# Kernel optimization log

Measured on AMD Instinct MI355X. Metric: run time of the kernel, lower is better.

Reference implementation:

```python
import jax, jax.numpy as jnp
import numpy as np

BLOCK_NUM = 64
B, M, K, N = 4, 4096, 4096, 4096  # batch, rows, in_features, out_features


def setup_inputs() -> dict:
    key = jax.random.key(0)
    k1, k2 = jax.random.split(key)
    x = jax.random.normal(k1, (B, M, K), dtype=jnp.float32)
    weight = jax.random.normal(k2, (K, N), dtype=jnp.float32) * 0.02
    return {"x": x, "weight": weight}


def reference(x, weight):
    # Block-local matmul: output block (i, j) = A_block(i, j) @ W_block(i, j).
    # No cross-block reduction: each (i, j) output block depends on exactly one
    # A block and one W block. Vectorized as a single einsum over all blocks.
    b, m, k = x.shape
    k2, n = weight.shape
    Bn = BLOCK_NUM
    r, c, o = m // Bn, k // Bn, n // Bn  # per-block rows / contract / cols
    A = x.reshape(b, Bn, r, Bn, c)        # [b, i, r, j, c]
    W = weight.reshape(Bn, c, Bn, o)      # [i, c, j, o] (rows split by i, cols by j)
    out = jnp.einsum('birjc,icjo->birjo', A, W)
    return out.reshape(b, m, n)
```

## Files before the change

### kernel.cpp

```cpp
#include <hip/hip_runtime.h>
#include <hip/hip_bf16.h>


typedef short bf16x8 __attribute__((ext_vector_type(8)));
typedef float f32x4 __attribute__((ext_vector_type(4)));

__device__ __forceinline__ unsigned short f2bf(float f) {
    union { float f; unsigned int u; } v; v.f = f;
    unsigned int u = v.u;
    u += 0x7fffu + ((u >> 16) & 1u);
    return (unsigned short)(u >> 16);
}

__global__ __launch_bounds__(256, 4) void block_matmul_kernel(
    const float* __restrict__ x, const float* __restrict__ w,
    float* __restrict__ out) {
    __shared__ unsigned short As[64 * 64];
    __shared__ unsigned short Ws[64 * 64];

    const int nwg   = 4 * 64 * 64;
    const int chunk = nwg >> 3;
    int orig = blockIdx.x;
    int wg   = (orig & 7) * chunk + (orig >> 3);

    int b  = wg & 3;
    int ij = wg >> 2;
    int i  = ij >> 6;
    int j  = ij & 63;

    const float* Ab = x   + ((size_t)b * 4096 + (size_t)i * 64) * 4096 + (size_t)j * 64;
    const float* Wb = w   + ((size_t)i * 64) * 4096 + (size_t)j * 64;
    float*       Ob = out + ((size_t)b * 4096 + (size_t)i * 64) * 4096 + (size_t)j * 64;

    const int t = threadIdx.x;

    #pragma unroll
    for (int it = 0; it < 4; ++it) {
        int idx = it * 256 + t;
        int m   = idx >> 4;
        int k4  = (idx & 15) << 2;
        float4 v = *reinterpret_cast<const float4*>(Ab + (size_t)m * 4096 + k4);
        unsigned long long pk =
            (unsigned long long)f2bf(v.x)        |
            ((unsigned long long)f2bf(v.y) << 16) |
            ((unsigned long long)f2bf(v.z) << 32) |
            ((unsigned long long)f2bf(v.w) << 48);
        int addr = m * 128 + ((k4 * 2) ^ ((m & 7) << 4));
        *reinterpret_cast<unsigned long long*>(reinterpret_cast<char*>(As) + addr) = pk;
    }

    {
        int n  = t & 63;
        int kq = (t >> 6) << 2;
        #pragma unroll
        for (int it = 0; it < 4; ++it) {
            int kb = it * 16 + kq;
            float f0 = Wb[(size_t)(kb + 0) * 4096 + n];
            float f1 = Wb[(size_t)(kb + 1) * 4096 + n];
            float f2 = Wb[(size_t)(kb + 2) * 4096 + n];
            float f3 = Wb[(size_t)(kb + 3) * 4096 + n];
            unsigned long long pk =
                (unsigned long long)f2bf(f0)        |
                ((unsigned long long)f2bf(f1) << 16) |
                ((unsigned long long)f2bf(f2) << 32) |
                ((unsigned long long)f2bf(f3) << 48);
            int addr = n * 128 + ((kb * 2) ^ ((n & 7) << 4));
            *reinterpret_cast<unsigned long long*>(reinterpret_cast<char*>(Ws) + addr) = pk;
        }
    }

    __syncthreads();

    const int l  = t & 63;
    const int wv = t >> 6;
    const int lr = l & 15;
    const int lk = l >> 4;

    f32x4 acc[4] = {{0.f,0.f,0.f,0.f},{0.f,0.f,0.f,0.f},
                    {0.f,0.f,0.f,0.f},{0.f,0.f,0.f,0.f}};

    #pragma unroll
    for (int kt = 0; kt < 2; ++kt) {
        int kbyte = kt * 64 + lk * 16;
        int am = wv * 16 + lr;
        bf16x8 af = *reinterpret_cast<const bf16x8*>(
            reinterpret_cast<const char*>(As) + am * 128 + (kbyte ^ ((am & 7) << 4)));
        #pragma unroll
        for (int nt = 0; nt < 4; ++nt) {
            int bn = nt * 16 + lr;
            bf16x8 bfr = *reinterpret_cast<const bf16x8*>(
                reinterpret_cast<const char*>(Ws) + bn * 128 + (kbyte ^ ((bn & 7) << 4)));
            acc[nt] = __builtin_amdgcn_mfma_f32_16x16x32_bf16(af, bfr, acc[nt], 0, 0, 0);
        }
    }

    #pragma unroll
    for (int nt = 0; nt < 4; ++nt) {
        #pragma unroll
        for (int r = 0; r < 4; ++r) {
            int orow = wv * 16 + lk * 4 + r;
            int ocol = nt * 16 + lr;
            Ob[(size_t)orow * 4096 + ocol] = acc[nt][r];
        }
    }
}

extern "C" void kernel_launch(void* const* d_in, const int* in_sizes, int n_in,
                              void* d_out, int out_size, void* d_ws, size_t ws_size,
                              hipStream_t stream) {
    const float* x = (const float*)d_in[0];
    const float* w = (const float*)d_in[1];
    float* out = (float*)d_out;

    dim3 grid(4 * 64 * 64);
    dim3 block(256);
    block_matmul_kernel<<<grid, block, 0, stream>>>(x, w, out);
}
```

Measured before the change: 143.5 us.

## Process two column blocks per workgroup and stage output through LDS for vector stores

Each workgroup now handles two adjacent j blocks (128 columns), which doubles the width of each row segment it reads and halves the grid. The output is written to shared memory with a swizzle and then stored with float4 writes covering 512-byte row segments, replacing scattered scalar stores. The batch index moves to the outermost position in the block mapping, and launch bounds rise to 5 waves. The cost is 32KB of LDS per workgroup and two extra barriers, which may limit occupancy.

```diff
diff --git a/kernel.cpp b/kernel.cpp
--- a/kernel.cpp
+++ b/kernel.cpp
@@ -12,60 +12,61 @@
     return (unsigned short)(u >> 16);
 }
 
-__global__ __launch_bounds__(256, 4) void block_matmul_kernel(
+__global__ __launch_bounds__(256, 5) void block_matmul_kernel(
     const float* __restrict__ x, const float* __restrict__ w,
     float* __restrict__ out) {
-    __shared__ unsigned short As[64 * 64];
-    __shared__ unsigned short Ws[64 * 64];
+    __shared__ char smem[32768];
+    unsigned short* As = reinterpret_cast<unsigned short*>(smem);
+    unsigned short* Ws = reinterpret_cast<unsigned short*>(smem + 16384);
+    float*          Os = reinterpret_cast<float*>(smem);
 
-    const int nwg   = 4 * 64 * 64;
-    const int chunk = nwg >> 3;
+    const int chunk = 8192 >> 3;
     int orig = blockIdx.x;
     int wg   = (orig & 7) * chunk + (orig >> 3);
 
-    int b  = wg & 3;
-    int ij = wg >> 2;
-    int i  = ij >> 6;
-    int j  = ij & 63;
+    int b = wg >> 11;
+    int i = (wg >> 5) & 63;
+    int q = wg & 31;
 
-    const float* Ab = x   + ((size_t)b * 4096 + (size_t)i * 64) * 4096 + (size_t)j * 64;
-    const float* Wb = w   + ((size_t)i * 64) * 4096 + (size_t)j * 64;
-    float*       Ob = out + ((size_t)b * 4096 + (size_t)i * 64) * 4096 + (size_t)j * 64;
+    const float* Ab = x   + ((size_t)(b * 4096 + i * 64)) * 4096 + q * 128;
+    const float* Wb = w   + ((size_t)(i * 64)) * 4096 + q * 128;
+    float*       Ob = out + ((size_t)(b * 4096 + i * 64)) * 4096 + q * 128;
 
     const int t = threadIdx.x;
 
     #pragma unroll
-    for (int it = 0; it < 4; ++it) {
+    for (int it = 0; it < 8; ++it) {
         int idx = it * 256 + t;
-        int m   = idx >> 4;
-        int k4  = (idx & 15) << 2;
+        int m   = idx >> 5;
+        int k4  = (idx & 31) << 2;
         float4 v = *reinterpret_cast<const float4*>(Ab + (size_t)m * 4096 + k4);
         unsigned long long pk =
-            (unsigned long long)f2bf(v.x)        |
+            (unsigned long long)f2bf(v.x)         |
             ((unsigned long long)f2bf(v.y) << 16) |
             ((unsigned long long)f2bf(v.z) << 32) |
             ((unsigned long long)f2bf(v.w) << 48);
-        int addr = m * 128 + ((k4 * 2) ^ ((m & 7) << 4));
-        *reinterpret_cast<unsigned long long*>(reinterpret_cast<char*>(As) + addr) = pk;
+        int addr = m * 256 + ((k4 * 2) ^ ((m & 7) << 4));
+        *reinterpret_cast<unsigned long long*>(smem + addr) = pk;
     }
 
     {
-        int n  = t & 63;
-        int kq = (t >> 6) << 2;
+        int n  = t & 127;
+        int c0 = (t >> 7) << 2;
         #pragma unroll
-        for (int it = 0; it < 4; ++it) {
-            int kb = it * 16 + kq;
-            float f0 = Wb[(size_t)(kb + 0) * 4096 + n];
-            float f1 = Wb[(size_t)(kb + 1) * 4096 + n];
-            float f2 = Wb[(size_t)(kb + 2) * 4096 + n];
-            float f3 = Wb[(size_t)(kb + 3) * 4096 + n];
+        for (int it = 0; it < 8; ++it) {
+            int c = it * 8 + c0;
+            float f0 = Wb[(size_t)(c + 0) * 4096 + n];
+            float f1 = Wb[(size_t)(c + 1) * 4096 + n];
+            float f2 = Wb[(size_t)(c + 2) * 4096 + n];
+            float f3 = Wb[(size_t)(c + 3) * 4096 + n];
             unsigned long long pk =
-                (unsigned long long)f2bf(f0)        |
+                (unsigned long long)f2bf(f0)         |
                 ((unsigned long long)f2bf(f1) << 16) |
                 ((unsigned long long)f2bf(f2) << 32) |
                 ((unsigned long long)f2bf(f3) << 48);
-            int addr = n * 128 + ((kb * 2) ^ ((n & 7) << 4));
-            *reinterpret_cast<unsigned long long*>(reinterpret_cast<char*>(Ws) + addr) = pk;
+            int addr = n * 128 + ((c * 2) ^ ((n & 7) << 4));
+            *reinterpret_cast<unsigned long long*>(
+                reinterpret_cast<char*>(Ws) + addr) = pk;
         }
     }
 
@@ -76,32 +77,55 @@
     const int lr = l & 15;
     const int lk = l >> 4;
 
-    f32x4 acc[4] = {{0.f,0.f,0.f,0.f},{0.f,0.f,0.f,0.f},
-                    {0.f,0.f,0.f,0.f},{0.f,0.f,0.f,0.f}};
+    f32x4 acc[8];
+    #pragma unroll
+    for (int z = 0; z < 8; ++z) acc[z] = (f32x4){0.f, 0.f, 0.f, 0.f};
 
+    const int am = wv * 16 + lr;
     #pragma unroll
-    for (int kt = 0; kt < 2; ++kt) {
-        int kbyte = kt * 64 + lk * 16;
-        int am = wv * 16 + lr;
-        bf16x8 af = *reinterpret_cast<const bf16x8*>(
-            reinterpret_cast<const char*>(As) + am * 128 + (kbyte ^ ((am & 7) << 4)));
+    for (int jj = 0; jj < 2; ++jj) {
         #pragma unroll
-        for (int nt = 0; nt < 4; ++nt) {
-            int bn = nt * 16 + lr;
-            bf16x8 bfr = *reinterpret_cast<const bf16x8*>(
-                reinterpret_cast<const char*>(Ws) + bn * 128 + (kbyte ^ ((bn & 7) << 4)));
-            acc[nt] = __builtin_amdgcn_mfma_f32_16x16x32_bf16(af, bfr, acc[nt], 0, 0, 0);
+        for (int kt = 0; kt < 2; ++kt) {
+            int kbA = jj * 128 + kt * 64 + lk * 16;
+            bf16x8 af = *reinterpret_cast<const bf16x8*>(
+                smem + am * 256 + (kbA ^ ((am & 7) << 4)));
+            int kbB = kt * 64 + lk * 16;
+            #pragma unroll
+            for (int nt = 0; nt < 4; ++nt) {
+                int bn = jj * 64 + nt * 16 + lr;
+                bf16x8 bfr = *reinterpret_cast<const bf16x8*>(
+                    reinterpret_cast<const char*>(Ws) + bn * 128 +
+                    (kbB ^ ((bn & 7) << 4)));
+                acc[jj * 4 + nt] =
+                    __builtin_amdgcn_mfma_f32_16x16x32_bf16(af, bfr,
+                                                            acc[jj * 4 + nt],
+                                                            0, 0, 0);
+            }
         }
     }
 
+    __syncthreads();
+
     #pragma unroll
-    for (int nt = 0; nt < 4; ++nt) {
+    for (int fn = 0; fn < 8; ++fn) {
         #pragma unroll
         for (int r = 0; r < 4; ++r) {
-            int orow = wv * 16 + lk * 4 + r;
-            int ocol = nt * 16 + lr;
-            Ob[(size_t)orow * 4096 + ocol] = acc[nt][r];
+            int row = wv * 16 + lk * 4 + r;
+            int col = fn * 16 + lr;
+            Os[row * 128 + (col ^ ((row & 7) << 2))] = acc[fn][r];
         }
+    }
+
+    __syncthreads();
+
+    #pragma unroll
+    for (int it = 0; it < 8; ++it) {
+        int idx = it * 256 + t;
+        int row = idx >> 5;
+        int c4  = (idx & 31) << 2;
+        int col = c4 ^ ((row & 7) << 2);
+        f32x4 v = *reinterpret_cast<const f32x4*>(Os + row * 128 + col);
+        *reinterpret_cast<f32x4*>(Ob + (size_t)row * 4096 + c4) = v;
     }
 }
 
@@ -112,7 +136,7 @@
     const float* w = (const float*)d_in[1];
     float* out = (float*)d_out;
 
-    dim3 grid(4 * 64 * 64);
+    dim3 grid(8192);
     dim3 block(256);
     block_matmul_kernel<<<grid, block, 0, stream>>>(x, w, out);
 }
```

After: 123.9 us. 13.6% less time.

## Reuse each weight block across batch and pipeline loads in persistent-style workgroups

Applied to the files above, without the earlier changes.

Each workgroup now handles one block-row i and four consecutive block-columns across all four batches: 1024 workgroups in place of 16384. Every converted W block in LDS is reused for all batches. A fragments go straight from global memory into registers, skipping LDS, and loads are prefetched one phase ahead. The weight tiles are double-buffered in LDS so the next W block's global loads and bf16 conversion overlap with MFMA work on the current one. The cost is more registers per thread and fewer, longer workgroups, which may reduce latency hiding on a kernel bound by memory bandwidth.

```diff
diff --git a/kernel.cpp b/kernel.cpp
--- a/kernel.cpp
+++ b/kernel.cpp
@@ -12,97 +12,140 @@
     return (unsigned short)(u >> 16);
 }
 
+__device__ __forceinline__ bf16x8 pack8(float4 a, float4 b) {
+    bf16x8 r;
+    r[0] = (short)f2bf(a.x); r[1] = (short)f2bf(a.y);
+    r[2] = (short)f2bf(a.z); r[3] = (short)f2bf(a.w);
+    r[4] = (short)f2bf(b.x); r[5] = (short)f2bf(b.y);
+    r[6] = (short)f2bf(b.z); r[7] = (short)f2bf(b.w);
+    return r;
+}
+
+#define BSTRIDE 16777216
+
 __global__ __launch_bounds__(256, 4) void block_matmul_kernel(
     const float* __restrict__ x, const float* __restrict__ w,
     float* __restrict__ out) {
-    __shared__ unsigned short As[64 * 64];
-    __shared__ unsigned short Ws[64 * 64];
+    __shared__ char smem[16384];
 
-    const int nwg   = 4 * 64 * 64;
-    const int chunk = nwg >> 3;
     int orig = blockIdx.x;
-    int wg   = (orig & 7) * chunk + (orig >> 3);
+    int wg   = (orig & 7) * 128 + (orig >> 3);
+    int i = wg >> 4;
+    int s = wg & 15;
 
-    int b  = wg & 3;
-    int ij = wg >> 2;
-    int i  = ij >> 6;
-    int j  = ij & 63;
+    const int rowbase = i * 64;
+    const int colbase = s * 256;
 
-    const float* Ab = x   + ((size_t)b * 4096 + (size_t)i * 64) * 4096 + (size_t)j * 64;
-    const float* Wb = w   + ((size_t)i * 64) * 4096 + (size_t)j * 64;
-    float*       Ob = out + ((size_t)b * 4096 + (size_t)i * 64) * 4096 + (size_t)j * 64;
-
-    const int t = threadIdx.x;
-
-    #pragma unroll
-    for (int it = 0; it < 4; ++it) {
-        int idx = it * 256 + t;
-        int m   = idx >> 4;
-        int k4  = (idx & 15) << 2;
-        float4 v = *reinterpret_cast<const float4*>(Ab + (size_t)m * 4096 + k4);
-        unsigned long long pk =
-            (unsigned long long)f2bf(v.x)        |
-            ((unsigned long long)f2bf(v.y) << 16) |
-            ((unsigned long long)f2bf(v.z) << 32) |
-            ((unsigned long long)f2bf(v.w) << 48);
-        int addr = m * 128 + ((k4 * 2) ^ ((m & 7) << 4));
-        *reinterpret_cast<unsigned long long*>(reinterpret_cast<char*>(As) + addr) = pk;
-    }
-
-    {
-        int n  = t & 63;
-        int kq = (t >> 6) << 2;
-        #pragma unroll
-        for (int it = 0; it < 4; ++it) {
-            int kb = it * 16 + kq;
-            float f0 = Wb[(size_t)(kb + 0) * 4096 + n];
-            float f1 = Wb[(size_t)(kb + 1) * 4096 + n];
-            float f2 = Wb[(size_t)(kb + 2) * 4096 + n];
-            float f3 = Wb[(size_t)(kb + 3) * 4096 + n];
-            unsigned long long pk =
-                (unsigned long long)f2bf(f0)        |
-                ((unsigned long long)f2bf(f1) << 16) |
-                ((unsigned long long)f2bf(f2) << 32) |
-                ((unsigned long long)f2bf(f3) << 48);
-            int addr = n * 128 + ((kb * 2) ^ ((n & 7) << 4));
-            *reinterpret_cast<unsigned long long*>(reinterpret_cast<char*>(Ws) + addr) = pk;
-        }
-    }
-
-    __syncthreads();
-
+    const int t  = threadIdx.x;
     const int l  = t & 63;
     const int wv = t >> 6;
     const int lr = l & 15;
     const int lk = l >> 4;
+    const int am = wv * 16 + lr;
 
-    f32x4 acc[4] = {{0.f,0.f,0.f,0.f},{0.f,0.f,0.f,0.f},
-                    {0.f,0.f,0.f,0.f},{0.f,0.f,0.f,0.f}};
+    const int wn = t & 63;
+    const int cg = t >> 6;
 
-    #pragma unroll
-    for (int kt = 0; kt < 2; ++kt) {
-        int kbyte = kt * 64 + lk * 16;
-        int am = wv * 16 + lr;
-        bf16x8 af = *reinterpret_cast<const bf16x8*>(
-            reinterpret_cast<const char*>(As) + am * 128 + (kbyte ^ ((am & 7) << 4)));
-        #pragma unroll
-        for (int nt = 0; nt < 4; ++nt) {
-            int bn = nt * 16 + lr;
-            bf16x8 bfr = *reinterpret_cast<const bf16x8*>(
-                reinterpret_cast<const char*>(Ws) + bn * 128 + (kbyte ^ ((bn & 7) << 4)));
-            acc[nt] = __builtin_amdgcn_mfma_f32_16x16x32_bf16(af, bfr, acc[nt], 0, 0, 0);
-        }
+    const float* Wbase = w + (size_t)rowbase * 4096 + colbase;
+    const float* Abase = x + ((size_t)rowbase + am) * 4096 + colbase + lk * 8;
+    float*       Obase = out + (size_t)rowbase * 4096 + colbase;
+
+    float  wregA[16], wregB[16];
+    float4 abuf[4];
+    bf16x8 wf[8];
+
+#define ISSUE_W(SET, s_) {                                                    \
+    const float* Wp = Wbase + (s_) * 64;                                      \
+    _Pragma("unroll") for (int it = 0; it < 4; ++it) {                        \
+        int cb = it * 16 + cg * 4;                                            \
+        _Pragma("unroll") for (int r = 0; r < 4; ++r)                         \
+            SET[it * 4 + r] = Wp[(size_t)(cb + r) * 4096 + wn];               \
+    } }
+
+#define WRITE_W(SET, bufoff) {                                                \
+    _Pragma("unroll") for (int it = 0; it < 4; ++it) {                        \
+        int c = it * 16 + cg * 4;                                             \
+        unsigned long long pk =                                               \
+            (unsigned long long)f2bf(SET[it * 4 + 0])         |               \
+            ((unsigned long long)f2bf(SET[it * 4 + 1]) << 16) |               \
+            ((unsigned long long)f2bf(SET[it * 4 + 2]) << 32) |               \
+            ((unsigned long long)f2bf(SET[it * 4 + 3]) << 48);                \
+        *reinterpret_cast<unsigned long long*>(                               \
+            smem + (bufoff) + wn * 128 + ((c * 2) ^ ((wn & 7) << 4))) = pk;   \
+    } }
+
+#define ISSUE_A(b_, jj_) {                                                    \
+    const float* Ap = Abase + (size_t)(b_) * BSTRIDE + (jj_) * 64;            \
+    abuf[0] = *reinterpret_cast<const float4*>(Ap);                           \
+    abuf[1] = *reinterpret_cast<const float4*>(Ap + 4);                       \
+    abuf[2] = *reinterpret_cast<const float4*>(Ap + 32);                      \
+    abuf[3] = *reinterpret_cast<const float4*>(Ap + 36);                      \
     }
 
-    #pragma unroll
-    for (int nt = 0; nt < 4; ++nt) {
-        #pragma unroll
-        for (int r = 0; r < 4; ++r) {
-            int orow = wv * 16 + lk * 4 + r;
-            int ocol = nt * 16 + lr;
-            Ob[(size_t)orow * 4096 + ocol] = acc[nt][r];
-        }
+#define LOAD_WF(bufoff) {                                                     \
+    _Pragma("unroll") for (int kt = 0; kt < 2; ++kt)                          \
+    _Pragma("unroll") for (int nt = 0; nt < 4; ++nt) {                        \
+        int bn = nt * 16 + lr;                                                \
+        int kb = kt * 64 + lk * 16;                                           \
+        wf[kt * 4 + nt] = *reinterpret_cast<const bf16x8*>(                   \
+            smem + (bufoff) + bn * 128 + (kb ^ ((bn & 7) << 4)));             \
+    } }
+
+#define PHASE(jj_, b_, nb_, nj_, HASNEXT) {                                   \
+    bf16x8 af0 = pack8(abuf[0], abuf[1]);                                     \
+    bf16x8 af1 = pack8(abuf[2], abuf[3]);                                     \
+    if (HASNEXT) ISSUE_A(nb_, nj_);                                           \
+    f32x4 acc[4];                                                             \
+    _Pragma("unroll") for (int nt = 0; nt < 4; ++nt)                          \
+        acc[nt] = (f32x4){0.f, 0.f, 0.f, 0.f};                                \
+    _Pragma("unroll") for (int nt = 0; nt < 4; ++nt)                          \
+        acc[nt] = __builtin_amdgcn_mfma_f32_16x16x32_bf16(af0, wf[nt],        \
+                                                          acc[nt], 0, 0, 0);  \
+    _Pragma("unroll") for (int nt = 0; nt < 4; ++nt)                          \
+        acc[nt] = __builtin_amdgcn_mfma_f32_16x16x32_bf16(af1, wf[4 + nt],    \
+                                                          acc[nt], 0, 0, 0);  \
+    float* Op = Obase + (size_t)(b_) * BSTRIDE + (jj_) * 64;                  \
+    _Pragma("unroll") for (int nt = 0; nt < 4; ++nt)                          \
+    _Pragma("unroll") for (int r = 0; r < 4; ++r)                             \
+        Op[(size_t)(wv * 16 + lk * 4 + r) * 4096 + nt * 16 + lr]              \
+            = acc[nt][r];                                                     \
     }
+
+    ISSUE_W(wregA, 0);
+    ISSUE_A(0, 0);
+    ISSUE_W(wregB, 1);
+    WRITE_W(wregA, 0);
+    __syncthreads();
+
+    LOAD_WF(0);
+    PHASE(0, 0, 1, 0, 1);
+    PHASE(0, 1, 2, 0, 1);
+    WRITE_W(wregB, 8192); ISSUE_W(wregA, 2);
+    PHASE(0, 2, 3, 0, 1);
+    PHASE(0, 3, 0, 1, 1);
+    __syncthreads();
+
+    LOAD_WF(8192);
+    PHASE(1, 0, 1, 1, 1);
+    PHASE(1, 1, 2, 1, 1);
+    WRITE_W(wregA, 0); ISSUE_W(wregB, 3);
+    PHASE(1, 2, 3, 1, 1);
+    PHASE(1, 3, 0, 2, 1);
+    __syncthreads();
+
+    LOAD_WF(0);
+    PHASE(2, 0, 1, 2, 1);
+    PHASE(2, 1, 2, 2, 1);
+    WRITE_W(wregB, 8192);
+    PHASE(2, 2, 3, 2, 1);
+    PHASE(2, 3, 0, 3, 1);
+    __syncthreads();
+
+    LOAD_WF(8192);
+    PHASE(3, 0, 1, 3, 1);
+    PHASE(3, 1, 2, 3, 1);
+    PHASE(3, 2, 3, 3, 1);
+    PHASE(3, 3, 0, 0, 0);
 }
 
 extern "C" void kernel_launch(void* const* d_in, const int* in_sizes, int n_in,
@@ -112,7 +155,7 @@
     const float* w = (const float*)d_in[1];
     float* out = (float*)d_out;
 
-    dim3 grid(4 * 64 * 64);
+    dim3 grid(1024);
     dim3 block(256);
     block_matmul_kernel<<<grid, block, 0, stream>>>(x, w, out);
 }
```

New measurement: 132.8 us. -7.5%, faster.

## Reuse W tile across batches, double-buffer A loads, stage outputs through LDS

Applied to the files above, without the earlier changes.

Each workgroup now handles a 64x128 output strip covering two column blocks and loops over all 4 batch entries. The W tile is converted to bf16 once and reused across batches, with A loads for the next batch issued in registers while the current batch computes. Outputs are staged through a swizzled LDS buffer so global stores become 16-byte vectors. The grid shrinks to 2048 workgroups, LDS grows to 48KB and occupancy drops to 3, and per-wave register pressure is higher.

```diff
diff --git a/kernel.cpp b/kernel.cpp
--- a/kernel.cpp
+++ b/kernel.cpp
@@ -12,97 +12,136 @@
     return (unsigned short)(u >> 16);
 }
 
-__global__ __launch_bounds__(256, 4) void block_matmul_kernel(
+__device__ __forceinline__ unsigned long long pack4(float4 v) {
+    return  (unsigned long long)f2bf(v.x)        |
+           ((unsigned long long)f2bf(v.y) << 16) |
+           ((unsigned long long)f2bf(v.z) << 32) |
+           ((unsigned long long)f2bf(v.w) << 48);
+}
+
+#define BSTRIDE 16777216ull
+
+#define FENCE() asm volatile("s_waitcnt lgkmcnt(0)" ::: "memory")
+
+__global__ __launch_bounds__(256, 3) void block_matmul_kernel(
     const float* __restrict__ x, const float* __restrict__ w,
     float* __restrict__ out) {
-    __shared__ unsigned short As[64 * 64];
-    __shared__ unsigned short Ws[64 * 64];
+    __shared__ char smem[49152];
 
-    const int nwg   = 4 * 64 * 64;
-    const int chunk = nwg >> 3;
-    int orig = blockIdx.x;
-    int wg   = (orig & 7) * chunk + (orig >> 3);
-
-    int b  = wg & 3;
-    int ij = wg >> 2;
-    int i  = ij >> 6;
-    int j  = ij & 63;
-
-    const float* Ab = x   + ((size_t)b * 4096 + (size_t)i * 64) * 4096 + (size_t)j * 64;
-    const float* Wb = w   + ((size_t)i * 64) * 4096 + (size_t)j * 64;
-    float*       Ob = out + ((size_t)b * 4096 + (size_t)i * 64) * 4096 + (size_t)j * 64;
-
-    const int t = threadIdx.x;
-
-    #pragma unroll
-    for (int it = 0; it < 4; ++it) {
-        int idx = it * 256 + t;
-        int m   = idx >> 4;
-        int k4  = (idx & 15) << 2;
-        float4 v = *reinterpret_cast<const float4*>(Ab + (size_t)m * 4096 + k4);
-        unsigned long long pk =
-            (unsigned long long)f2bf(v.x)        |
-            ((unsigned long long)f2bf(v.y) << 16) |
-            ((unsigned long long)f2bf(v.z) << 32) |
-            ((unsigned long long)f2bf(v.w) << 48);
-        int addr = m * 128 + ((k4 * 2) ^ ((m & 7) << 4));
-        *reinterpret_cast<unsigned long long*>(reinterpret_cast<char*>(As) + addr) = pk;
-    }
-
-    {
-        int n  = t & 63;
-        int kq = (t >> 6) << 2;
-        #pragma unroll
-        for (int it = 0; it < 4; ++it) {
-            int kb = it * 16 + kq;
-            float f0 = Wb[(size_t)(kb + 0) * 4096 + n];
-            float f1 = Wb[(size_t)(kb + 1) * 4096 + n];
-            float f2 = Wb[(size_t)(kb + 2) * 4096 + n];
-            float f3 = Wb[(size_t)(kb + 3) * 4096 + n];
-            unsigned long long pk =
-                (unsigned long long)f2bf(f0)        |
-                ((unsigned long long)f2bf(f1) << 16) |
-                ((unsigned long long)f2bf(f2) << 32) |
-                ((unsigned long long)f2bf(f3) << 48);
-            int addr = n * 128 + ((kb * 2) ^ ((n & 7) << 4));
-            *reinterpret_cast<unsigned long long*>(reinterpret_cast<char*>(Ws) + addr) = pk;
-        }
-    }
-
-    __syncthreads();
-
+    const int t  = threadIdx.x;
     const int l  = t & 63;
     const int wv = t >> 6;
     const int lr = l & 15;
     const int lk = l >> 4;
 
-    f32x4 acc[4] = {{0.f,0.f,0.f,0.f},{0.f,0.f,0.f,0.f},
-                    {0.f,0.f,0.f,0.f},{0.f,0.f,0.f,0.f}};
+    int orig = blockIdx.x;
+    int wg   = (orig & 7) * 256 + (orig >> 3);
+    int i = wg >> 5;
+    int q = wg & 31;
+
+    const size_t rowbase = (size_t)i * 64;
+    const size_t colbase = (size_t)q * 128;
+
+    const float* Wb    = w   + rowbase * 4096 + colbase;
+    const float* Abase = x   + (rowbase + wv * 16) * 4096 + colbase;
+    float*       Obase = out + (rowbase + wv * 16) * 4096 + colbase;
+
+    char* Aslot = smem + 16384 + wv * 4096;
+    char* Bslot = smem + 32768 + wv * 4096;
+
+    const int wn = t & 127;
+    const int c0 = (t >> 7) << 2;
+    float wreg[32];
+    #pragma unroll
+    for (int it = 0; it < 8; ++it) {
+        int c = it * 8 + c0;
+        #pragma unroll
+        for (int r = 0; r < 4; ++r)
+            wreg[it * 4 + r] = Wb[(size_t)(c + r) * 4096 + wn];
+    }
+
+    const int rl0 = l >> 5;
+    const int u   = l & 31;
+    const float* Alane = Abase + (size_t)rl0 * 4096 + u * 4;
+
+#define LOADA(DST, b_) {                                                      \
+    const float* Ap = Alane + (size_t)(b_) * BSTRIDE;                         \
+    _Pragma("unroll") for (int s = 0; s < 8; ++s)                             \
+        DST[s] = *reinterpret_cast<const float4*>(Ap + (size_t)(s * 2) * 4096); }
+
+    float4 aA[8], aB[8];
+    LOADA(aA, 0);
+    LOADA(aB, 1);
 
     #pragma unroll
-    for (int kt = 0; kt < 2; ++kt) {
-        int kbyte = kt * 64 + lk * 16;
-        int am = wv * 16 + lr;
-        bf16x8 af = *reinterpret_cast<const bf16x8*>(
-            reinterpret_cast<const char*>(As) + am * 128 + (kbyte ^ ((am & 7) << 4)));
-        #pragma unroll
-        for (int nt = 0; nt < 4; ++nt) {
-            int bn = nt * 16 + lr;
-            bf16x8 bfr = *reinterpret_cast<const bf16x8*>(
-                reinterpret_cast<const char*>(Ws) + bn * 128 + (kbyte ^ ((bn & 7) << 4)));
-            acc[nt] = __builtin_amdgcn_mfma_f32_16x16x32_bf16(af, bfr, acc[nt], 0, 0, 0);
-        }
+    for (int it = 0; it < 8; ++it) {
+        int c = it * 8 + c0;
+        unsigned long long pk =
+            (unsigned long long)f2bf(wreg[it * 4 + 0])         |
+            ((unsigned long long)f2bf(wreg[it * 4 + 1]) << 16) |
+            ((unsigned long long)f2bf(wreg[it * 4 + 2]) << 32) |
+            ((unsigned long long)f2bf(wreg[it * 4 + 3]) << 48);
+        *reinterpret_cast<unsigned long long*>(
+            smem + wn * 128 + ((c * 2) ^ ((wn & 7) << 4))) = pk;
     }
 
-    #pragma unroll
-    for (int nt = 0; nt < 4; ++nt) {
-        #pragma unroll
-        for (int r = 0; r < 4; ++r) {
-            int orow = wv * 16 + lk * 4 + r;
-            int ocol = nt * 16 + lr;
-            Ob[(size_t)orow * 4096 + ocol] = acc[nt][r];
-        }
-    }
+    __syncthreads();
+
+#define STOREA(SRC) {                                                         \
+    _Pragma("unroll") for (int s = 0; s < 8; ++s) {                           \
+        int rl = s * 2 + rl0;                                                 \
+        *reinterpret_cast<unsigned long long*>(                               \
+            Aslot + rl * 256 + ((u * 8) ^ ((rl & 7) << 4))) = pack4(SRC[s]); } }
+
+#define BATCH(b_, CUR) {                                                      \
+    STOREA(CUR);                                                              \
+    if ((b_) < 2) LOADA(CUR, (b_) + 2);                                       \
+    FENCE();        \
+    _Pragma("unroll") for (int jj = 0; jj < 2; ++jj) {                        \
+        bf16x8 af0 = *reinterpret_cast<const bf16x8*>(                        \
+            Aslot + lr * 256 + ((jj * 128 + lk * 16) ^ ((lr & 7) << 4)));     \
+        bf16x8 af1 = *reinterpret_cast<const bf16x8*>(                        \
+            Aslot + lr * 256 + ((jj * 128 + 64 + lk * 16) ^ ((lr & 7) << 4)));\
+        f32x4 acc[4];                                                         \
+        _Pragma("unroll") for (int nt = 0; nt < 4; ++nt)                      \
+            acc[nt] = (f32x4){0.f, 0.f, 0.f, 0.f};                            \
+        _Pragma("unroll") for (int nt = 0; nt < 4; ++nt) {                    \
+            int bn = jj * 64 + nt * 16 + lr;                                  \
+            bf16x8 w0 = *reinterpret_cast<const bf16x8*>(                     \
+                smem + bn * 128 + ((lk * 16) ^ ((bn & 7) << 4)));             \
+            acc[nt] = __builtin_amdgcn_mfma_f32_16x16x32_bf16(                \
+                af0, w0, acc[nt], 0, 0, 0);                                   \
+        }                                                                     \
+        _Pragma("unroll") for (int nt = 0; nt < 4; ++nt) {                    \
+            int bn = jj * 64 + nt * 16 + lr;                                  \
+            bf16x8 w1 = *reinterpret_cast<const bf16x8*>(                     \
+                smem + bn * 128 + ((64 + lk * 16) ^ ((bn & 7) << 4)));        \
+            acc[nt] = __builtin_amdgcn_mfma_f32_16x16x32_bf16(                \
+                af1, w1, acc[nt], 0, 0, 0);                                   \
+        }                                                                     \
+        FENCE();       \
+        _Pragma("unroll") for (int nt = 0; nt < 4; ++nt)                      \
+        _Pragma("unroll") for (int r = 0; r < 4; ++r) {                       \
+            int brow = lk * 4 + r;                                            \
+            *reinterpret_cast<float*>(                                        \
+                Bslot + brow * 256 +                                          \
+                (((nt * 16 + lr) * 4) ^ ((brow & 7) << 4))) = acc[nt][r];     \
+        }                                                                     \
+        FENCE();                  \
+        float* Ob = Obase + (size_t)(b_) * BSTRIDE + jj * 64;                 \
+        _Pragma("unroll") for (int s2 = 0; s2 < 4; ++s2) {                    \
+            int row = s2 * 4 + lk;                                            \
+            int u2  = l & 15;                                                 \
+            f32x4 v = *reinterpret_cast<const f32x4*>(                        \
+                Bslot + row * 256 + ((u2 * 16) ^ ((row & 7) << 4)));          \
+            *reinterpret_cast<f32x4*>(Ob + (size_t)row * 4096 + u2 * 4) = v;  \
+        }                                                                     \
+    } }
+
+    BATCH(0, aA);
+    BATCH(1, aB);
+    BATCH(2, aA);
+    BATCH(3, aB);
 }
 
 extern "C" void kernel_launch(void* const* d_in, const int* in_sizes, int n_in,
@@ -112,7 +151,7 @@
     const float* w = (const float*)d_in[1];
     float* out = (float*)d_out;
 
-    dim3 grid(4 * 64 * 64);
+    dim3 grid(2048);
     dim3 block(256);
     block_matmul_kernel<<<grid, block, 0, stream>>>(x, w, out);
 }
```

Measured after the change: 120.4 us. 16.1% less time.
